# Performance work log

Hardware: AMD Instinct MI355X
Metric: run time of the kernel (lower is better)

## Reference

```python
import jax, jax.numpy as jnp
import numpy as np

B, S, D = 4, 2048, 2048
E = 8
H = (4 * D) // E  # per-expert hidden = 1024
DS = D // 2       # shared-layer hidden
LOAD_BALANCE_WEIGHT = 0.01


def setup_inputs() -> dict:
    key = jax.random.key(0)
    ks = jax.random.split(key, 12)
    s = 0.02
    return {
        "x": jax.random.normal(ks[0], (B, S, D), dtype=jnp.float32),
        "W_router": jax.random.normal(ks[1], (D, E), dtype=jnp.float32) * s,
        "b_router": jnp.zeros((E,), dtype=jnp.float32),
        "W1": jax.random.normal(ks[2], (E, D, H), dtype=jnp.float32) * s,
        "b1": jnp.zeros((E, H), dtype=jnp.float32),
        "W2": jax.random.normal(ks[3], (E, H, D), dtype=jnp.float32) * s,
        "b2": jnp.zeros((E, D), dtype=jnp.float32),
        "Ws1": jax.random.normal(ks[4], (D, DS), dtype=jnp.float32) * s,
        "bs1": jnp.zeros((DS,), dtype=jnp.float32),
        "Ws2": jax.random.normal(ks[5], (DS, D), dtype=jnp.float32) * s,
        "bs2": jnp.zeros((D,), dtype=jnp.float32),
    }


def reference(x, W_router, b_router, W1, b1, W2, b2, Ws1, bs1, Ws2, bs2):
    # Router: soft weights over all experts (soft-MoE, every expert runs).
    router_logits = jnp.einsum("bsd,de->bse", x, W_router) + b_router
    router_weights = jax.nn.softmax(router_logits, axis=-1)  # (B,S,E)

    # Shared branch: Linear -> GELU (exact, matching torch default) -> Linear.
    shared = jax.nn.gelu(jnp.einsum("bsd,dh->bsh", x, Ws1) + bs1, approximate=False)
    shared = jnp.einsum("bsh,hd->bsd", shared, Ws2) + bs2

    # All experts as one batched GEMM pair (fuses the torch Python loop).
    h = jax.nn.gelu(jnp.einsum("bsd,edh->bseh", x, W1) + b1, approximate=False)  # (B,S,E,H)
    expert_out = jnp.einsum("bseh,ehd->bsed", h, W2) + b2  # (B,S,E,D)

    # Softmax-weighted combine + scaled shared residual (dropout=0 / eval).
    weighted = jnp.einsum("bsed,bse->bsd", expert_out, router_weights)
    output = weighted + 0.1 * shared

    # Load-balance aux loss: MSE between mean usage and uniform.
    expert_usage = router_weights.mean(axis=(0, 1))  # (E,)
    uniform = jnp.full_like(expert_usage, 1.0 / E)
    aux_loss = jnp.mean((expert_usage - uniform) ** 2) * LOAD_BALANCE_WEIGHT
    return output, aux_loss
```

## Files before the change

kernel.cpp:

```cpp
#include <hip/hip_runtime.h>
#include <hip/hip_bf16.h>
#include <stdint.h>

#define DEV static __device__ __forceinline__

typedef __attribute__((ext_vector_type(4))) float f32x4;
typedef __attribute__((ext_vector_type(8))) short bf16x8;
typedef __attribute__((ext_vector_type(4))) float float4v;

constexpr int NBATCH = 4;
constexpr int SEQ    = 2048;
constexpr int DIM    = 2048;
constexpr int NEXP   = 8;
constexpr int HEXP   = 1024;
constexpr int DSH    = 1024;
constexpr int NTOK   = NBATCH * SEQ;
constexpr int JEXP   = NEXP * HEXP;
constexpr int JTOT   = JEXP + DSH;

DEV short f2bf(float f) {
  __hip_bfloat16 b = __float2bfloat16(f);
  union { __hip_bfloat16 b; short s; } u; u.b = b; return u.s;
}

DEV void gload16(const void* gp, const void* lp) {
  __builtin_amdgcn_global_load_lds(
      (__attribute__((address_space(1))) void*)(uintptr_t)gp,
      (__attribute__((address_space(3))) void*)(uint32_t)(uintptr_t)lp,
      16, 0, 0);
}

__global__ void conv_x_k(const float* __restrict__ x, short* __restrict__ xb) {
  size_t i = (size_t)blockIdx.x * blockDim.x + threadIdx.x;
  const float4v* s = reinterpret_cast<const float4v*>(x) + i * 2;
  float4v a = s[0], b = s[1];
  bf16x8 o;
  o[0] = f2bf(a.x); o[1] = f2bf(a.y); o[2] = f2bf(a.z); o[3] = f2bf(a.w);
  o[4] = f2bf(b.x); o[5] = f2bf(b.y); o[6] = f2bf(b.z); o[7] = f2bf(b.w);
  *reinterpret_cast<bf16x8*>(xb + i * 8) = o;
}

__global__ __launch_bounds__(256) void router_k(
    const float* __restrict__ x, const float* __restrict__ Wr,
    const float* __restrict__ br, float* __restrict__ rw,
    float* __restrict__ auxs) {
  const int wave = threadIdx.x >> 6, lane = threadIdx.x & 63;
  const int t = blockIdx.x * 4 + wave;
  const float* xr = x + (size_t)t * DIM;
  float a[NEXP];
#pragma unroll
  for (int e = 0; e < NEXP; ++e) a[e] = 0.f;
  for (int i = 0; i < DIM / 64; ++i) {
    int k = i * 64 + lane;
    float xv = xr[k];
    const float* w = Wr + (size_t)k * NEXP;
#pragma unroll
    for (int e = 0; e < NEXP; ++e) a[e] = fmaf(xv, w[e], a[e]);
  }
#pragma unroll
  for (int e = 0; e < NEXP; ++e) {
    float v = a[e];
#pragma unroll
    for (int off = 32; off > 0; off >>= 1) v += __shfl_xor(v, off, 64);
    a[e] = v + br[e];
  }
  float mx = a[0];
#pragma unroll
  for (int e = 1; e < NEXP; ++e) mx = fmaxf(mx, a[e]);
  float s = 0.f;
#pragma unroll
  for (int e = 0; e < NEXP; ++e) { a[e] = expf(a[e] - mx); s += a[e]; }
  float inv = 1.f / s;
#pragma unroll
  for (int e = 0; e < NEXP; ++e) a[e] *= inv;
  if (lane == 0) {
#pragma unroll
    for (int e = 0; e < NEXP; ++e) rw[(size_t)t * NEXP + e] = a[e];
  }
  __shared__ float blk[NEXP];
  if (threadIdx.x < NEXP) blk[threadIdx.x] = 0.f;
  __syncthreads();
  if (lane == 0) {
#pragma unroll
    for (int e = 0; e < NEXP; ++e) atomicAdd(&blk[e], a[e]);
  }
  __syncthreads();
  if (threadIdx.x < NEXP) atomicAdd(&auxs[threadIdx.x], blk[threadIdx.x]);
}

__global__ void zero_aux_k(float* auxs) {
  if (threadIdx.x < NEXP) auxs[threadIdx.x] = 0.f;
}

__global__ void fin_aux_k(const float* __restrict__ auxs, float* __restrict__ dst) {
  if (threadIdx.x == 0) {
    float s = 0.f;
    for (int e = 0; e < NEXP; ++e) {
      float u = auxs[e] / (float)NTOK - (1.0f / NEXP);
      s += u * u;
    }
    dst[0] = (s / NEXP) * 0.01f;
  }
}

__global__ __launch_bounds__(256) void conv_w1_k(
    const float* __restrict__ W1, const float* __restrict__ Ws1,
    short* __restrict__ dst, int jbase, int jc) {
  __shared__ float tile[64][65];
  const int j0 = jbase + blockIdx.x * 64;
  const int k0 = blockIdx.y * 64;
  const int tx = threadIdx.x & 63;
  const int ty = threadIdx.x >> 6;
#pragma unroll
  for (int i = 0; i < 16; ++i) {
    int kk = ty * 16 + i;
    int j = j0 + tx, k = k0 + kk;
    float v;
    if (j < JEXP) {
      int e = j >> 10, h = j & 1023;
      v = W1[(size_t)e * DIM * HEXP + (size_t)k * HEXP + h];
    } else {
      v = Ws1[(size_t)k * DSH + (j - JEXP)];
    }
    tile[kk][tx] = v;
  }
  __syncthreads();
#pragma unroll
  for (int i = 0; i < 16; ++i) {
    int jj = ty * 16 + i;
    int jloc = j0 - jbase + jj;
    dst[(size_t)jloc * DIM + k0 + tx] = f2bf(tile[tx][jj]);
  }
}

__global__ __launch_bounds__(256) void conv_w2_k(
    const float* __restrict__ W2, const float* __restrict__ Ws2,
    short* __restrict__ dst, int jbase, int jc) {
  __shared__ float tile[64][65];
  const int j0 = jbase + blockIdx.x * 64;
  const int d0 = blockIdx.y * 64;
  const int tx = threadIdx.x & 63;
  const int ty = threadIdx.x >> 6;
#pragma unroll
  for (int i = 0; i < 16; ++i) {
    int jj = ty * 16 + i;
    int j = j0 + jj;
    float v;
    if (j < JEXP) {
      int e = j >> 10, h = j & 1023;
      v = W2[(size_t)e * HEXP * DIM + (size_t)h * DIM + d0 + tx];
    } else {
      v = 0.1f * Ws2[(size_t)(j - JEXP) * DIM + d0 + tx];
    }
    tile[jj][tx] = v;
  }
  __syncthreads();
#pragma unroll
  for (int i = 0; i < 16; ++i) {
    int dd = ty * 16 + i;
    dst[(size_t)(d0 + dd) * jc + (j0 - jbase) + tx] = f2bf(tile[tx][dd]);
  }
}

template <int MODE>
__global__ __launch_bounds__(512, 2) void gemm256(
    const short* __restrict__ A, const short* __restrict__ Bt, int K,
    const float* __restrict__ rw,
    const float* __restrict__ bias_a, const float* __restrict__ bias_b,
    short* __restrict__ hOut, int jbase, int jc,
    float* __restrict__ out, int nx) {
  extern __shared__ short smem[];
  short* As = smem;
  short* Bs = smem + 32768;

  const int tid = threadIdx.x;
  const int w = tid >> 6, lane = tid & 63;
  const int wr = w >> 2, wc = w & 3;

  const int nwg = nx * (NTOK / 256);
  int orig = blockIdx.x;
  const int q = nwg >> 3, r = nwg & 7;
  const int xcd = orig & 7, off = orig >> 3;
  const int bid = (xcd < r ? xcd * (q + 1) : r * (q + 1) + (xcd - r) * q) + off;
  const int bx = bid % nx, by = bid / nx;
  const int m0 = by * 256, n0 = bx * 256;

  f32x4 acc[8][4] = {};

  const int aoff = ((lane & 15) << 6) + ((((lane >> 4) ^ ((lane >> 1) & 3)) & 3) << 4);
  const char* Abase = (const char*)As + wr * 8192 + aoff;
  const char* Bbase = (const char*)Bs + wc * 4096 + aoff;

  const int srow = lane >> 2;
  const int scol = (((lane & 3) ^ ((lane >> 3) & 3)) << 3);
  const short* gA0 = A + (size_t)(m0 + w * 32 + srow) * K + scol;
  const short* gB0 = Bt + (size_t)(n0 + w * 32 + srow) * K + scol;
  const size_t k16 = (size_t)16 * K;
  short* lA = As + w * 1024;
  short* lB = Bs + w * 1024;
  const int NT = K >> 5;

#define STG_A(TT) { const int sl_ = (TT) & 3; const size_t co_ = (size_t)(TT) << 5; \
    gload16(gA0 + co_, lA + sl_ * 8192);                                           \
    gload16(gA0 + k16 + co_, lA + sl_ * 8192 + 512); }
#define STG_B(TT) { const int sl_ = (TT) & 3; const size_t co_ = (size_t)(TT) << 5; \
    gload16(gB0 + co_, lB + sl_ * 8192);                                           \
    gload16(gB0 + k16 + co_, lB + sl_ * 8192 + 512); }

  STG_A(0); STG_B(0); STG_A(1); STG_B(1); STG_A(2); STG_B(2);
  asm volatile("s_waitcnt vmcnt(8)" ::: "memory");
  __builtin_amdgcn_s_barrier();
  __builtin_amdgcn_sched_barrier(0);

  bf16x8 bc[4], a03[4], a47[4], bn[4], a03n[4];
#pragma unroll
  for (int i = 0; i < 4; ++i) bc[i]  = *(const bf16x8*)(Bbase + i * 1024);
#pragma unroll
  for (int i = 0; i < 4; ++i) a03[i] = *(const bf16x8*)(Abase + i * 1024);

  for (int t = 0; t < NT; ++t) {
    const char* pa = Abase + (size_t)(t & 3) * 16384;
#pragma unroll
    for (int i = 0; i < 4; ++i) a47[i] = *(const bf16x8*)(pa + 4096 + i * 1024);
    if (t <= NT - 3) { asm volatile("s_waitcnt vmcnt(4)" ::: "memory"); }
    else             { asm volatile("s_waitcnt vmcnt(0)" ::: "memory"); }
    __builtin_amdgcn_s_barrier();
    __builtin_amdgcn_sched_barrier(0);
    if (t + 3 < NT) STG_A(t + 3);
    if (t + 1 < NT) {
      const char* pan = Abase + (size_t)((t + 1) & 3) * 16384;
      const char* pbn = Bbase + (size_t)((t + 1) & 3) * 16384;
#pragma unroll
      for (int i = 0; i < 4; ++i) bn[i]   = *(const bf16x8*)(pbn + i * 1024);
#pragma unroll
      for (int i = 0; i < 4; ++i) a03n[i] = *(const bf16x8*)(pan + i * 1024);
      asm volatile("s_waitcnt lgkmcnt(8)" ::: "memory");
    } else {
      asm volatile("s_waitcnt lgkmcnt(0)" ::: "memory");
    }
    __builtin_amdgcn_sched_barrier(0);
    __builtin_amdgcn_s_setprio(1);
#pragma unroll
    for (int mi = 0; mi < 4; ++mi)
#pragma unroll
      for (int ni = 0; ni < 4; ++ni)
        acc[mi][ni] = __builtin_amdgcn_mfma_f32_16x16x32_bf16(a03[mi], bc[ni], acc[mi][ni], 0, 0, 0);
    if (t + 3 < NT) STG_B(t + 3);
#pragma unroll
    for (int mi = 0; mi < 4; ++mi)
#pragma unroll
      for (int ni = 0; ni < 4; ++ni)
        acc[mi + 4][ni] = __builtin_amdgcn_mfma_f32_16x16x32_bf16(a47[mi], bc[ni], acc[mi + 4][ni], 0, 0, 0);
    __builtin_amdgcn_s_setprio(0);
#pragma unroll
    for (int i = 0; i < 4; ++i) { bc[i] = bn[i]; a03[i] = a03n[i]; }
  }
#undef STG_A
#undef STG_B

  const int r0 = (lane >> 4) * 4;
  const int ccol = lane & 15;
#pragma unroll
  for (int m = 0; m < 8; ++m) {
#pragma unroll
    for (int i = 0; i < 4; ++i) {
      const int trow = m0 + wr * 128 + m * 16 + r0 + i;
      if (MODE == 0) {
#pragma unroll
        for (int n = 0; n < 4; ++n) {
          const int col = n0 + wc * 64 + n * 16 + ccol;
          const int j = jbase + col;
          float v = acc[m][n][i];
          float bias = (j < JEXP) ? bias_a[j] : bias_b[j - JEXP];
          float val = v + bias;
          float g = 0.5f * val * (1.0f + erff(val * 0.70710678118654752f));
          float wgt = (j < JEXP) ? rw[(size_t)trow * NEXP + (j >> 10)] : 1.0f;
          hOut[(size_t)trow * jc + col] = f2bf(g * wgt);
        }
      } else if (MODE == 1) {
        float rw8[8];
#pragma unroll
        for (int e = 0; e < 8; ++e) rw8[e] = rw[(size_t)trow * NEXP + e];
#pragma unroll
        for (int n = 0; n < 4; ++n) {
          const int col = n0 + wc * 64 + n * 16 + ccol;
          float bias = 0.1f * bias_b[col];
#pragma unroll
          for (int e = 0; e < 8; ++e) bias += rw8[e] * bias_a[(size_t)e * DIM + col];
          out[(size_t)trow * DIM + col] = acc[m][n][i] + bias;
        }
      } else {
#pragma unroll
        for (int n = 0; n < 4; ++n) {
          const int col = n0 + wc * 64 + n * 16 + ccol;
          out[(size_t)trow * DIM + col] += acc[m][n][i];
        }
      }
    }
  }
}

template <int MODE>
__global__ __launch_bounds__(256) void gemm128(
    const short* __restrict__ A, const short* __restrict__ Bt, int K,
    const float* __restrict__ rw,
    const float* __restrict__ bias_a, const float* __restrict__ bias_b,
    short* __restrict__ hOut, int jbase, int jc,
    float* __restrict__ out) {
  __shared__ short As[128 * 64];
  __shared__ short Bs[128 * 64];
  const int tid = threadIdx.x;
  const int wave = tid >> 6, lane = tid & 63;
  const int wr = wave >> 1, wc = wave & 1;
  const int m0 = blockIdx.y * 128;
  const int n0 = blockIdx.x * 128;

  f32x4 acc[4][4] = {};

  const int srow = wave * 8 + (lane >> 3);
  const int scol = (((lane & 7) ^ (lane >> 3)) << 3);
  const short* gA = A + (size_t)(m0 + srow) * K + scol;
  const short* gB = Bt + (size_t)(n0 + srow) * K + scol;
  const short* lA = As + wave * 512;
  const short* lB = Bs + wave * 512;

  const int rrow = lane & 15;
  const int koff = lane >> 4;
  const int kxor = lane & 7;

  for (int kt = 0; kt < K; kt += 64) {
#pragma unroll
    for (int i = 0; i < 4; ++i) {
      gload16(gA + (size_t)i * 32 * K + kt, lA + i * 2048);
      gload16(gB + (size_t)i * 32 * K + kt, lB + i * 2048);
    }
    asm volatile("s_waitcnt vmcnt(0)" ::: "memory");
    __syncthreads();
#pragma unroll
    for (int kk = 0; kk < 2; ++kk) {
      bf16x8 af[4], bfv[4];
#pragma unroll
      for (int m = 0; m < 4; ++m) {
        int row = wr * 64 + m * 16 + rrow;
        int chunk = (kk * 4 + koff) ^ kxor;
        af[m] = *reinterpret_cast<const bf16x8*>(&As[row * 64 + chunk * 8]);
      }
#pragma unroll
      for (int n = 0; n < 4; ++n) {
        int row = wc * 64 + n * 16 + rrow;
        int chunk = (kk * 4 + koff) ^ kxor;
        bfv[n] = *reinterpret_cast<const bf16x8*>(&Bs[row * 64 + chunk * 8]);
      }
#pragma unroll
      for (int m = 0; m < 4; ++m)
#pragma unroll
        for (int n = 0; n < 4; ++n)
          acc[m][n] = __builtin_amdgcn_mfma_f32_16x16x32_bf16(af[m], bfv[n], acc[m][n], 0, 0, 0);
    }
    __syncthreads();
  }

  const int r0 = (lane >> 4) * 4;
  const int ccol = lane & 15;
#pragma unroll
  for (int m = 0; m < 4; ++m) {
#pragma unroll
    for (int n = 0; n < 4; ++n) {
      int col = n0 + wc * 64 + n * 16 + ccol;
#pragma unroll
      for (int i = 0; i < 4; ++i) {
        int t = m0 + wr * 64 + m * 16 + r0 + i;
        float v = acc[m][n][i];
        if (MODE == 0) {
          int j = jbase + col;
          float bias = (j < JEXP) ? bias_a[j] : bias_b[j - JEXP];
          float val = v + bias;
          float g = 0.5f * val * (1.0f + erff(val * 0.70710678118654752f));
          float wg = (j < JEXP) ? rw[(size_t)t * NEXP + (j >> 10)] : 1.0f;
          hOut[(size_t)t * jc + col] = f2bf(g * wg);
        } else if (MODE == 1) {
          float bias = 0.1f * bias_b[col];
#pragma unroll
          for (int e = 0; e < NEXP; ++e)
            bias += rw[(size_t)t * NEXP + e] * bias_a[(size_t)e * DIM + col];
          out[(size_t)t * DIM + col] = v + bias;
        } else {
          out[(size_t)t * DIM + col] += v;
        }
      }
    }
  }
}

extern "C" void kernel_launch(void* const* d_in, const int* in_sizes, int n_in,
                              void* d_out, int out_size, void* d_ws, size_t ws_size,
                              hipStream_t stream) {
  const float* x   = (const float*)d_in[0];
  const float* Wr  = (const float*)d_in[1];
  const float* br  = (const float*)d_in[2];
  const float* W1  = (const float*)d_in[3];
  const float* b1  = (const float*)d_in[4];
  const float* W2  = (const float*)d_in[5];
  const float* b2  = (const float*)d_in[6];
  const float* Ws1 = (const float*)d_in[7];
  const float* bs1 = (const float*)d_in[8];
  const float* Ws2 = (const float*)d_in[9];
  const float* bs2 = (const float*)d_in[10];
  float* out = (float*)d_out;

  char* wsb = (char*)d_ws;
  short* xb   = (short*)wsb;
  float* rw   = (float*)(wsb + 33554432);
  float* auxs = (float*)(wsb + 33816576);
  const size_t need_fixed = 33816832ull;

  const int jcands[8] = {9216, 4608, 3072, 2304, 1536, 768, 512, 256};
  int jc = 256;
  for (int ci = 0; ci < 8; ++ci) {
    if (need_fixed + (size_t)jcands[ci] * 24576ull <= ws_size) { jc = jcands[ci]; break; }
  }
  const int nc = JTOT / jc;
  short* w1t  = (short*)(wsb + need_fixed);
  short* w2t  = w1t + (size_t)jc * DIM;
  short* hbuf = w2t + (size_t)DIM * jc;

  bool big = true;
  {
    auto* f0 = gemm256<0>; auto* f1 = gemm256<1>; auto* f2 = gemm256<2>;
    if (hipFuncSetAttribute(reinterpret_cast<const void*>(f0),
                            hipFuncAttributeMaxDynamicSharedMemorySize, 131072) != hipSuccess) big = false;
    if (hipFuncSetAttribute(reinterpret_cast<const void*>(f1),
                            hipFuncAttributeMaxDynamicSharedMemorySize, 131072) != hipSuccess) big = false;
    if (hipFuncSetAttribute(reinterpret_cast<const void*>(f2),
                            hipFuncAttributeMaxDynamicSharedMemorySize, 131072) != hipSuccess) big = false;
  }

  zero_aux_k<<<1, 64, 0, stream>>>(auxs);
  conv_x_k<<<(NTOK * DIM / 8) / 256, 256, 0, stream>>>(x, xb);
  router_k<<<NTOK / 4, 256, 0, stream>>>(x, Wr, br, rw, auxs);
  fin_aux_k<<<1, 64, 0, stream>>>(auxs, out + (size_t)NTOK * DIM);

  for (int c = 0; c < nc; ++c) {
    const int jbase = c * jc;
    conv_w1_k<<<dim3(jc / 64, DIM / 64), 256, 0, stream>>>(W1, Ws1, w1t, jbase, jc);
    conv_w2_k<<<dim3(jc / 64, DIM / 64), 256, 0, stream>>>(W2, Ws2, w2t, jbase, jc);
    if (big) {
      const int nx1 = jc / 256, ny = NTOK / 256;
      gemm256<0><<<nx1 * ny, 512, 131072, stream>>>(
          xb, w1t, DIM, rw, b1, bs1, hbuf, jbase, jc, nullptr, nx1);
      const int nx2 = DIM / 256;
      if (c == 0) {
        gemm256<1><<<nx2 * ny, 512, 131072, stream>>>(
            hbuf, w2t, jc, rw, b2, bs2, nullptr, 0, jc, out, nx2);
      } else {
        gemm256<2><<<nx2 * ny, 512, 131072, stream>>>(
            hbuf, w2t, jc, rw, nullptr, nullptr, nullptr, 0, jc, out, nx2);
      }
    } else {
      gemm128<0><<<dim3(jc / 128, NTOK / 128), 256, 0, stream>>>(
          xb, w1t, DIM, rw, b1, bs1, hbuf, jbase, jc, nullptr);
      if (c == 0) {
        gemm128<1><<<dim3(DIM / 128, NTOK / 128), 256, 0, stream>>>(
            hbuf, w2t, jc, rw, b2, bs2, nullptr, 0, jc, out);
      } else {
        gemm128<2><<<dim3(DIM / 128, NTOK / 128), 256, 0, stream>>>(
            hbuf, w2t, jc, rw, nullptr, nullptr, nullptr, 0, jc, out);
      }
    }
  }
}
```

Before: 976.1 us.

## Unroll GEMM main loop by four with ping-pong register buffers and compiler scheduling

Unrolls the K loop of the 256x256 bf16 MFMA GEMM by four, alternating two register buffer sets instead of copying next-tile fragments each iteration, and uses constant LDS slot offsets. It removes the explicit sched_barrier, setprio and lgkmcnt waits, letting the compiler interleave next-tile LDS reads with the first MFMA half. The peeled epilogue assumes NT is a multiple of four and at least four. Dropping the manual scheduling controls risks worse instruction ordering or register pressure.

```diff
diff --git a/kernel.cpp b/kernel.cpp
--- a/kernel.cpp
+++ b/kernel.cpp
@@ -161,6 +161,8 @@
     dst[(size_t)(d0 + dd) * jc + (j0 - jbase) + tx] = f2bf(tile[tx][dd]);
   }
 }
+
+#define BARRIER_F() { asm volatile("" ::: "memory"); __builtin_amdgcn_s_barrier(); asm volatile("" ::: "memory"); }
 
 template <int MODE>
 __global__ __launch_bounds__(512, 2) void gemm256(
@@ -207,54 +209,54 @@
     gload16(gB0 + co_, lB + sl_ * 8192);                                           \
     gload16(gB0 + k16 + co_, lB + sl_ * 8192 + 512); }
 
+#define TILE_BODY(T, SL, BCC, A03C, BCN, A03N, STAGE_OK, VM)                       \
+  {                                                                                \
+    const char* pa_ = Abase + (SL) * 16384;                                        \
+    _Pragma("unroll") for (int i = 0; i < 4; ++i)                                  \
+      a47[i] = *(const bf16x8*)(pa_ + 4096 + i * 1024);                            \
+    asm volatile("s_waitcnt vmcnt(" #VM ")" ::: "memory");                         \
+    BARRIER_F();                                                                   \
+    if (STAGE_OK) { STG_A((T) + 3); }                                              \
+    _Pragma("unroll") for (int mi = 0; mi < 4; ++mi)                               \
+      _Pragma("unroll") for (int ni = 0; ni < 4; ++ni)                             \
+        acc[mi][ni] = __builtin_amdgcn_mfma_f32_16x16x32_bf16(A03C[mi], BCC[ni], acc[mi][ni], 0, 0, 0); \
+    if ((T) + 1 < NT) {                                                            \
+      const char* pan_ = Abase + (((SL) + 1) & 3) * 16384;                         \
+      const char* pbn_ = Bbase + (((SL) + 1) & 3) * 16384;                         \
+      _Pragma("unroll") for (int i = 0; i < 4; ++i)                                \
+        BCN[i] = *(const bf16x8*)(pbn_ + i * 1024);                                \
+      _Pragma("unroll") for (int i = 0; i < 4; ++i)                                \
+        A03N[i] = *(const bf16x8*)(pan_ + i * 1024);                               \
+    }                                                                              \
+    if (STAGE_OK) { STG_B((T) + 3); }                                              \
+    _Pragma("unroll") for (int mi = 0; mi < 4; ++mi)                               \
+      _Pragma("unroll") for (int ni = 0; ni < 4; ++ni)                             \
+        acc[mi + 4][ni] = __builtin_amdgcn_mfma_f32_16x16x32_bf16(a47[mi], BCC[ni], acc[mi + 4][ni], 0, 0, 0); \
+  }
+
   STG_A(0); STG_B(0); STG_A(1); STG_B(1); STG_A(2); STG_B(2);
   asm volatile("s_waitcnt vmcnt(8)" ::: "memory");
-  __builtin_amdgcn_s_barrier();
-  __builtin_amdgcn_sched_barrier(0);
-
-  bf16x8 bc[4], a03[4], a47[4], bn[4], a03n[4];
-#pragma unroll
-  for (int i = 0; i < 4; ++i) bc[i]  = *(const bf16x8*)(Bbase + i * 1024);
-#pragma unroll
-  for (int i = 0; i < 4; ++i) a03[i] = *(const bf16x8*)(Abase + i * 1024);
-
-  for (int t = 0; t < NT; ++t) {
-    const char* pa = Abase + (size_t)(t & 3) * 16384;
-#pragma unroll
-    for (int i = 0; i < 4; ++i) a47[i] = *(const bf16x8*)(pa + 4096 + i * 1024);
-    if (t <= NT - 3) { asm volatile("s_waitcnt vmcnt(4)" ::: "memory"); }
-    else             { asm volatile("s_waitcnt vmcnt(0)" ::: "memory"); }
-    __builtin_amdgcn_s_barrier();
-    __builtin_amdgcn_sched_barrier(0);
-    if (t + 3 < NT) STG_A(t + 3);
-    if (t + 1 < NT) {
-      const char* pan = Abase + (size_t)((t + 1) & 3) * 16384;
-      const char* pbn = Bbase + (size_t)((t + 1) & 3) * 16384;
-#pragma unroll
-      for (int i = 0; i < 4; ++i) bn[i]   = *(const bf16x8*)(pbn + i * 1024);
-#pragma unroll
-      for (int i = 0; i < 4; ++i) a03n[i] = *(const bf16x8*)(pan + i * 1024);
-      asm volatile("s_waitcnt lgkmcnt(8)" ::: "memory");
-    } else {
-      asm volatile("s_waitcnt lgkmcnt(0)" ::: "memory");
-    }
-    __builtin_amdgcn_sched_barrier(0);
-    __builtin_amdgcn_s_setprio(1);
-#pragma unroll
-    for (int mi = 0; mi < 4; ++mi)
-#pragma unroll
-      for (int ni = 0; ni < 4; ++ni)
-        acc[mi][ni] = __builtin_amdgcn_mfma_f32_16x16x32_bf16(a03[mi], bc[ni], acc[mi][ni], 0, 0, 0);
-    if (t + 3 < NT) STG_B(t + 3);
-#pragma unroll
-    for (int mi = 0; mi < 4; ++mi)
-#pragma unroll
-      for (int ni = 0; ni < 4; ++ni)
-        acc[mi + 4][ni] = __builtin_amdgcn_mfma_f32_16x16x32_bf16(a47[mi], bc[ni], acc[mi + 4][ni], 0, 0, 0);
-    __builtin_amdgcn_s_setprio(0);
-#pragma unroll
-    for (int i = 0; i < 4; ++i) { bc[i] = bn[i]; a03[i] = a03n[i]; }
-  }
+  BARRIER_F();
+
+  bf16x8 bc0[4], a030[4], bc1[4], a031[4], a47[4];
+#pragma unroll
+  for (int i = 0; i < 4; ++i) bc0[i]  = *(const bf16x8*)(Bbase + i * 1024);
+#pragma unroll
+  for (int i = 0; i < 4; ++i) a030[i] = *(const bf16x8*)(Abase + i * 1024);
+
+  int t = 0;
+  for (; t + 7 < NT; t += 4) {
+    TILE_BODY(t + 0, 0, bc0, a030, bc1, a031, true, 4)
+    TILE_BODY(t + 1, 1, bc1, a031, bc0, a030, true, 4)
+    TILE_BODY(t + 2, 2, bc0, a030, bc1, a031, true, 4)
+    TILE_BODY(t + 3, 3, bc1, a031, bc0, a030, true, 4)
+  }
+  TILE_BODY(NT - 4, 0, bc0, a030, bc1, a031, true,  4)
+  TILE_BODY(NT - 3, 1, bc1, a031, bc0, a030, false, 4)
+  TILE_BODY(NT - 2, 2, bc0, a030, bc1, a031, false, 0)
+  TILE_BODY(NT - 1, 3, bc1, a031, bc0, a030, false, 0)
+
+#undef TILE_BODY
 #undef STG_A
 #undef STG_B
 
```

Result: faster. 953.4 us (-2.3%).
